# Kernel tuning notes

Measured on AMD Instinct MI355X. Metric: run time of the kernel, lower is better.

## Reference

```python
import jax, jax.numpy as jnp
import numpy as np

R = 16      # box filter radius (init kwarg)
EPS = 1e-4  # regularization (init kwarg)


def _diff_x(src, r):
    c = jnp.cumsum(src, axis=-2)
    left = c[..., r:2 * r + 1, :]
    middle = c[..., 2 * r + 1:, :] - c[..., :-2 * r - 1, :]
    right = c[..., -1:, :] - c[..., -2 * r - 1:-r - 1, :]
    return jnp.concatenate([left, middle, right], axis=-2)


def _diff_y(src, r):
    c = jnp.cumsum(src, axis=-1)
    left = c[..., r:2 * r + 1]
    middle = c[..., 2 * r + 1:] - c[..., :-2 * r - 1]
    right = c[..., -1:] - c[..., -2 * r - 1:-r - 1]
    return jnp.concatenate([left, middle, right], axis=-1)


def boxfilter2d(src, radius):
    return _diff_y(_diff_x(src, radius), radius)


def guidedfilter2d_color(guide, src, radius, eps):
    # guide: (B,3,H,W), src: (B,C,H,W)
    g_r, g_g, g_b = guide[:, 0:1], guide[:, 1:2], guide[:, 2:3]
    ones = jnp.ones_like(g_r)
    N = boxfilter2d(ones, radius)                       # (B,1,H,W)
    mean_I = boxfilter2d(guide, radius) / N             # (B,3,H,W)
    mI_r, mI_g, mI_b = mean_I[:, 0:1], mean_I[:, 1:2], mean_I[:, 2:3]
    mean_p = boxfilter2d(src, radius) / N               # (B,C,H,W)
    mean_Ip_r = boxfilter2d(g_r * src, radius) / N
    mean_Ip_g = boxfilter2d(g_g * src, radius) / N
    mean_Ip_b = boxfilter2d(g_b * src, radius) / N
    cov_Ip_r = mean_Ip_r - mI_r * mean_p
    cov_Ip_g = mean_Ip_g - mI_g * mean_p
    cov_Ip_b = mean_Ip_b - mI_b * mean_p
    v_rr = boxfilter2d(g_r * g_r, radius) / N - mI_r * mI_r + eps
    v_rg = boxfilter2d(g_r * g_g, radius) / N - mI_r * mI_g
    v_rb = boxfilter2d(g_r * g_b, radius) / N - mI_r * mI_b
    v_gg = boxfilter2d(g_g * g_g, radius) / N - mI_g * mI_g + eps
    v_gb = boxfilter2d(g_g * g_b, radius) / N - mI_g * mI_b
    v_bb = boxfilter2d(g_b * g_b, radius) / N - mI_b * mI_b + eps
    det = (v_rr * v_gg * v_bb + v_rg * v_gb * v_rb + v_rb * v_rg * v_gb
           - v_rb * v_gg * v_rb - v_rg * v_rg * v_bb - v_rr * v_gb * v_gb)
    i_rr = (v_gg * v_bb - v_gb * v_gb) / det
    i_rg = -(v_rg * v_bb - v_rb * v_gb) / det
    i_rb = (v_rg * v_gb - v_rb * v_gg) / det
    i_gg = (v_rr * v_bb - v_rb * v_rb) / det
    i_gb = -(v_rr * v_gb - v_rb * v_rg) / det
    i_bb = (v_rr * v_gg - v_rg * v_rg) / det
    # inv_sigma: (B,3,3,H,W) per-pixel inverse covariance
    inv_sigma = jnp.stack([
        jnp.stack([i_rr, i_rg, i_rb], axis=1),
        jnp.stack([i_rg, i_gg, i_gb], axis=1),
        jnp.stack([i_rb, i_gb, i_bb], axis=1)], axis=1)[..., 0, :, :]
    cov_Ip = jnp.stack([cov_Ip_r, cov_Ip_g, cov_Ip_b], axis=1)  # (B,3,C,H,W)
    a = jnp.einsum('bichw,bijhw->bjchw', cov_Ip, inv_sigma)     # (B,3,C,H,W)
    b = mean_p - a[:, 0] * mI_r - a[:, 1] * mI_g - a[:, 2] * mI_b
    mean_a = boxfilter2d(a, radius) / N[:, None]                # (B,3,C,H,W)
    mean_b = boxfilter2d(b, radius) / N
    q = jnp.einsum('bichw,bihw->bchw', mean_a, guide) + mean_b
    return q


def setup_inputs() -> dict:
    key = jax.random.key(0)
    k1, k2 = jax.random.split(key)
    guide = jax.random.uniform(k1, (1, 3, 2048, 2048), dtype=jnp.float32)
    src = jax.random.uniform(k2, (1, 3, 2048, 2048), dtype=jnp.float32)
    return {"guide": guide, "src": src}


def reference(guide, src):
    return guidedfilter2d_color(guide, src, R, EPS)
```

## Files before the change

### kernel.cpp

```cpp
#include <hip/hip_runtime.h>
#include <cstdio>
#include <cstdint>

#define HH 2048
#define WWI 2048
#define RAD 16
#define EPSF 1e-4f
#define BRA 16
#define BRB 32
#define W_OUT 94

typedef _Float16 h16;
constexpr size_t PLN = (size_t)HH * WWI;
constexpr int ROWB = WWI * 4;

__device__ __forceinline__ int cnt1d(int p, int n) {
    int lo = p - RAD; if (lo < 0) lo = 0;
    int hi = p + RAD; if (hi > n - 1) hi = n - 1;
    return hi - lo + 1;
}

__device__ __forceinline__ float ldf(const float* __restrict__ p, int boff) {
    return *reinterpret_cast<const float*>(reinterpret_cast<const char*>(p) + boff);
}
__device__ __forceinline__ float2 ldf2(const float* __restrict__ p, int boff) {
    return *reinterpret_cast<const float2*>(reinterpret_cast<const char*>(p) + boff);
}
__device__ __forceinline__ uint32_t ldu(const uint32_t* __restrict__ p, int boff) {
    return *reinterpret_cast<const uint32_t*>(reinterpret_cast<const char*>(p) + boff);
}
__device__ __forceinline__ void stu2(uint32_t* __restrict__ p, int boff, uint2 v) {
    *reinterpret_cast<uint2*>(reinterpret_cast<char*>(p) + boff) = v;
}
__device__ __forceinline__ void stf(float* __restrict__ p, int boff, float v) {
    *reinterpret_cast<float*>(reinterpret_cast<char*>(p) + boff) = v;
}
__device__ __forceinline__ uint32_t pk(float a, float b) {
    union { h16 h[2]; uint32_t u; } t;
    t.h[0] = (h16)a; t.h[1] = (h16)b; return t.u;
}
__device__ __forceinline__ float2 upk(uint32_t u) {
    union { uint32_t u; h16 h[2]; } t; t.u = u;
    return make_float2((float)t.h[0], (float)t.h[1]);
}

template<int CTRL, int RM>
__device__ __forceinline__ float dpp_add(float x) {
    int t = __builtin_amdgcn_update_dpp(0, __builtin_bit_cast(int, x), CTRL, RM, 0xf, false);
    return x + __builtin_bit_cast(float, t);
}
__device__ __forceinline__ float wscan(float x) {
    x = dpp_add<0x111, 0xf>(x);
    x = dpp_add<0x112, 0xf>(x);
    x = dpp_add<0x114, 0xf>(x);
    x = dpp_add<0x118, 0xf>(x);
    x = dpp_add<0x142, 0xa>(x);
    x = dpp_add<0x143, 0xc>(x);
    return x;
}
__device__ __forceinline__ float bperm(int byteaddr, float v) {
    return __builtin_bit_cast(float,
        __builtin_amdgcn_ds_bpermute(byteaddr, __builtin_bit_cast(int, v)));
}

template<bool ADD>
__device__ __forceinline__ void prod21(float v0, float v1, float v2,
                                       float v3, float v4, float v5, float S[21]) {
    float p[21];
    p[0] = v0; p[1] = v1; p[2] = v2; p[3] = v3; p[4] = v4; p[5] = v5;
    p[6] = v0 * v3; p[7] = v0 * v4; p[8] = v0 * v5;
    p[9] = v1 * v3; p[10] = v1 * v4; p[11] = v1 * v5;
    p[12] = v2 * v3; p[13] = v2 * v4; p[14] = v2 * v5;
    p[15] = v0 * v0; p[16] = v0 * v1; p[17] = v0 * v2;
    p[18] = v1 * v1; p[19] = v1 * v2; p[20] = v2 * v2;
#pragma unroll
    for (int c = 0; c < 21; ++c) { if constexpr (ADD) S[c] += p[c]; else S[c] -= p[c]; }
}

template<bool ADD>
__device__ __forceinline__ void acc21p(const float* __restrict__ g0, const float* __restrict__ g1,
                                       const float* __restrict__ g2, const float* __restrict__ s0,
                                       const float* __restrict__ s1, const float* __restrict__ s2,
                                       int boff, bool ok, float S0[21], float S1[21]) {
    if (!ok) return;
    const float2 a0 = ldf2(g0, boff), a1 = ldf2(g1, boff), a2 = ldf2(g2, boff);
    const float2 b0 = ldf2(s0, boff), b1 = ldf2(s1, boff), b2 = ldf2(s2, boff);
    prod21<ADD>(a0.x, a1.x, a2.x, b0.x, b1.x, b2.x, S0);
    prod21<ADD>(a0.y, a1.y, a2.y, b0.y, b1.y, b2.y, S1);
}

template<bool ADD>
__device__ __forceinline__ void acc12(const uint32_t* __restrict__ a0, const uint32_t* __restrict__ a1,
                                      const uint32_t* __restrict__ a2, const uint32_t* __restrict__ a3,
                                      const uint32_t* __restrict__ a4, const uint32_t* __restrict__ a5,
                                      int boff, bool ok, float S[12]) {
    if (!ok) return;
    const uint32_t u0 = ldu(a0, boff), u1 = ldu(a1, boff), u2 = ldu(a2, boff);
    const uint32_t u3 = ldu(a3, boff), u4 = ldu(a4, boff), u5 = ldu(a5, boff);
    const float2 f0 = upk(u0), f1 = upk(u1), f2 = upk(u2);
    const float2 f3 = upk(u3), f4 = upk(u4), f5 = upk(u5);
    if constexpr (ADD) {
        S[0] += f0.x; S[1] += f0.y; S[2] += f1.x; S[3] += f1.y;
        S[4] += f2.x; S[5] += f2.y; S[6] += f3.x; S[7] += f3.y;
        S[8] += f4.x; S[9] += f4.y; S[10] += f5.x; S[11] += f5.y;
    } else {
        S[0] -= f0.x; S[1] -= f0.y; S[2] -= f1.x; S[3] -= f1.y;
        S[4] -= f2.x; S[5] -= f2.y; S[6] -= f3.x; S[7] -= f3.y;
        S[8] -= f4.x; S[9] -= f4.y; S[10] -= f5.x; S[11] -= f5.y;
    }
}

__device__ __forceinline__ void solve_ab(const float S[21], float rN, float o[12]) {
    const float m0 = S[0] * rN, m1 = S[1] * rN, m2 = S[2] * rN;
    const float p0 = S[3] * rN, p1 = S[4] * rN, p2 = S[5] * rN;
    const float c00 = S[6] * rN - m0 * p0;
    const float c01 = S[7] * rN - m0 * p1;
    const float c02 = S[8] * rN - m0 * p2;
    const float c10 = S[9] * rN - m1 * p0;
    const float c11 = S[10] * rN - m1 * p1;
    const float c12 = S[11] * rN - m1 * p2;
    const float c20 = S[12] * rN - m2 * p0;
    const float c21 = S[13] * rN - m2 * p1;
    const float c22 = S[14] * rN - m2 * p2;
    const float vrr = S[15] * rN - m0 * m0 + EPSF;
    const float vrg = S[16] * rN - m0 * m1;
    const float vrb = S[17] * rN - m0 * m2;
    const float vgg = S[18] * rN - m1 * m1 + EPSF;
    const float vgb = S[19] * rN - m1 * m2;
    const float vbb = S[20] * rN - m2 * m2 + EPSF;
    const float det = vrr * vgg * vbb + vrg * vgb * vrb + vrb * vrg * vgb
                    - vrb * vgg * vrb - vrg * vrg * vbb - vrr * vgb * vgb;
    const float id = __builtin_amdgcn_rcpf(det);
    const float irr =  (vgg * vbb - vgb * vgb) * id;
    const float irg = -(vrg * vbb - vrb * vgb) * id;
    const float irb =  (vrg * vgb - vrb * vgg) * id;
    const float igg =  (vrr * vbb - vrb * vrb) * id;
    const float igb = -(vrr * vgb - vrb * vrg) * id;
    const float ibb =  (vrr * vgg - vrg * vrg) * id;
    const float a00 = c00 * irr + c10 * irg + c20 * irb;
    const float a01 = c01 * irr + c11 * irg + c21 * irb;
    const float a02 = c02 * irr + c12 * irg + c22 * irb;
    const float a10 = c00 * irg + c10 * igg + c20 * igb;
    const float a11 = c01 * irg + c11 * igg + c21 * igb;
    const float a12 = c02 * irg + c12 * igg + c22 * igb;
    const float a20 = c00 * irb + c10 * igb + c20 * ibb;
    const float a21 = c01 * irb + c11 * igb + c21 * ibb;
    const float a22 = c02 * irb + c12 * igb + c22 * ibb;
    o[0] = a00; o[1] = a01; o[2] = a02;
    o[3] = a10; o[4] = a11; o[5] = a12;
    o[6] = a20; o[7] = a21; o[8] = a22;
    o[9]  = p0 - a00 * m0 - a10 * m1 - a20 * m2;
    o[10] = p1 - a01 * m0 - a11 * m1 - a21 * m2;
    o[11] = p2 - a02 * m0 - a12 * m1 - a22 * m2;
}

#define LOAD6F(P, bo) { P[0] = ldf2(g0, bo); P[1] = ldf2(g1, bo); P[2] = ldf2(g2, bo); \
                        P[3] = ldf2(s0, bo); P[4] = ldf2(s1, bo); P[5] = ldf2(s2, bo); }
#define LOAD6U(P, bo) { P[0] = ldu(a0, bo); P[1] = ldu(a1, bo); P[2] = ldu(a2, bo); \
                        P[3] = ldu(a3, bo); P[4] = ldu(a4, bo); P[5] = ldu(a5, bo); }

__global__ __launch_bounds__(128, 3) void kA(const float* __restrict__ g,
                                             const float* __restrict__ s,
                                             uint32_t* __restrict__ ab) {
    const int lane = threadIdx.x & 63;
    const int wv   = blockIdx.x * 2 + (threadIdx.x >> 6);
    const int W0   = wv * W_OUT;
    const int X0   = W0 - 18;
    const int col0 = X0 + 2 * lane;
    const bool okc = (unsigned)col0 < (unsigned)WWI;
    const int r0   = blockIdx.y * BRA;
    const int aP17 = ((lane + 17) & 63) * 4;
    const int aP1  = ((lane + 1) & 63) * 4;
    const int j0   = W0 + 2 * lane;
    const bool outl = (lane <= 46) && (j0 < WWI);

    const float* g0 = g;         const float* g1 = g + PLN;   const float* g2 = g + 2 * PLN;
    const float* s0 = s;         const float* s1 = s + PLN;   const float* s2 = s + 2 * PLN;
    uint32_t* a0 = ab;           uint32_t* a1 = ab + PLN;     uint32_t* a2 = ab + 2 * PLN;
    uint32_t* a3 = ab + 3 * PLN; uint32_t* a4 = ab + 4 * PLN; uint32_t* a5 = ab + 5 * PLN;

    float S0[21], S1[21];
#pragma unroll
    for (int c = 0; c < 21; ++c) { S0[c] = 0.f; S1[c] = 0.f; }
    {
        int lo = r0 - RAD; if (lo < 0) lo = 0;
        int hi = r0 + RAD; if (hi > HH - 1) hi = HH - 1;
        int r = lo;
        if (okc) {
            int boff = lo * ROWB + col0 * 4;
            for (; r + 3 <= hi; r += 4) {
                float2 R0[6], R1[6], R2[6], R3[6];
                LOAD6F(R0, boff);
                LOAD6F(R1, boff + ROWB);
                LOAD6F(R2, boff + 2 * ROWB);
                LOAD6F(R3, boff + 3 * ROWB);
                prod21<true>(R0[0].x, R0[1].x, R0[2].x, R0[3].x, R0[4].x, R0[5].x, S0);
                prod21<true>(R0[0].y, R0[1].y, R0[2].y, R0[3].y, R0[4].y, R0[5].y, S1);
                prod21<true>(R1[0].x, R1[1].x, R1[2].x, R1[3].x, R1[4].x, R1[5].x, S0);
                prod21<true>(R1[0].y, R1[1].y, R1[2].y, R1[3].y, R1[4].y, R1[5].y, S1);
                prod21<true>(R2[0].x, R2[1].x, R2[2].x, R2[3].x, R2[4].x, R2[5].x, S0);
                prod21<true>(R2[0].y, R2[1].y, R2[2].y, R2[3].y, R2[4].y, R2[5].y, S1);
                prod21<true>(R3[0].x, R3[1].x, R3[2].x, R3[3].x, R3[4].x, R3[5].x, S0);
                prod21<true>(R3[0].y, R3[1].y, R3[2].y, R3[3].y, R3[4].y, R3[5].y, S1);
                boff += 4 * ROWB;
            }
            for (; r <= hi; ++r) {
                float2 R0[6];
                LOAD6F(R0, boff);
                prod21<true>(R0[0].x, R0[1].x, R0[2].x, R0[3].x, R0[4].x, R0[5].x, S0);
                prod21<true>(R0[0].y, R0[1].y, R0[2].y, R0[3].y, R0[4].y, R0[5].y, S1);
                boff += ROWB;
            }
        }
    }
    const float cx0 = (float)cnt1d(j0, WWI);
    const float cx1 = (float)cnt1d(j0 + 1, WWI);
    int raOff = (r0 + RAD + 1) * ROWB + col0 * 4;
    int rsOff = (r0 - RAD) * ROWB + col0 * 4;
    int oOff  = r0 * ROWB + j0 * 4;
    for (int ii = 0; ii < BRA; ++ii) {
        const int i = r0 + ii;
        float H0[21], H1[21];
#pragma unroll
        for (int c = 0; c < 21; ++c) {
            const float PP  = wscan(S0[c] + S1[c]);
            const float ppa = bperm(aP17, PP);
            const float s1b = bperm(aP17, S1[c]);
            const float s0b = bperm(aP1,  S0[c]);
            const float D = ppa - PP;
            H0[c] = D - s1b;
            H1[c] = D - s0b;
        }
        const float cy = (float)cnt1d(i, HH);
        float o0[12], o1[12];
        solve_ab(H0, __builtin_amdgcn_rcpf(cx0 * cy), o0);
        solve_ab(H1, __builtin_amdgcn_rcpf(cx1 * cy), o1);
        if (outl) {
            stu2(a0, oOff, make_uint2(pk(o0[0],  o0[1]),  pk(o1[0],  o1[1])));
            stu2(a1, oOff, make_uint2(pk(o0[2],  o0[3]),  pk(o1[2],  o1[3])));
            stu2(a2, oOff, make_uint2(pk(o0[4],  o0[5]),  pk(o1[4],  o1[5])));
            stu2(a3, oOff, make_uint2(pk(o0[6],  o0[7]),  pk(o1[6],  o1[7])));
            stu2(a4, oOff, make_uint2(pk(o0[8],  o0[9]),  pk(o1[8],  o1[9])));
            stu2(a5, oOff, make_uint2(pk(o0[10], o0[11]), pk(o1[10], o1[11])));
        }
        if (ii + 1 < BRA) {
            if (i + RAD + 1 < HH) acc21p<true >(g0, g1, g2, s0, s1, s2, raOff, okc, S0, S1);
            if (i - RAD >= 0)     acc21p<false>(g0, g1, g2, s0, s1, s2, rsOff, okc, S0, S1);
        }
        raOff += ROWB; rsOff += ROWB; oOff += ROWB;
    }
}

__global__ __launch_bounds__(256) void kB(const uint32_t* __restrict__ ab,
                                          const float* __restrict__ g,
                                          float* __restrict__ outp) {
    const int lane = threadIdx.x & 63;
    const int wv   = blockIdx.x * 4 + (threadIdx.x >> 6);
    const int x0   = wv * 32;
    const int col  = x0 - RAD + lane;
    const bool okc = (unsigned)col < (unsigned)WWI;
    const int colb = (okc ? col : 0) * 4;
    const int r0   = blockIdx.y * BRB;
    const int addrA = ((lane + 16) & 63) * 4;
    const int addrB = (lane >= 17 ? lane - 17 : 0) * 4;
    const bool subok = lane >= 17;
    const bool outl  = (lane >= 16) && (lane < 48);

    const uint32_t* a0 = ab;           const uint32_t* a1 = ab + PLN;     const uint32_t* a2 = ab + 2 * PLN;
    const uint32_t* a3 = ab + 3 * PLN; const uint32_t* a4 = ab + 4 * PLN; const uint32_t* a5 = ab + 5 * PLN;
    const float* g0 = g;  const float* g1 = g + PLN;  const float* g2 = g + 2 * PLN;
    float* o0 = outp;     float* o1 = outp + PLN;     float* o2 = outp + 2 * PLN;

    float S[12];
#pragma unroll
    for (int c = 0; c < 12; ++c) S[c] = 0.f;
    {
        int lo = r0 - RAD; if (lo < 0) lo = 0;
        int hi = r0 + RAD; if (hi > HH - 1) hi = HH - 1;
        int boff = lo * ROWB + col * 4;
        for (int r = lo; r <= hi; ++r) {
            acc12<true>(a0, a1, a2, a3, a4, a5, boff, okc, S);
            boff += ROWB;
        }
    }
    const float cx = (float)cnt1d(col, WWI);
    int oOff = r0 * ROWB + col * 4;

    uint32_t UA[6], UB[6], UA2[6], UB2[6];
    {
        const int boA = min(r0 + RAD + 1, HH - 1) * ROWB + colb;
        const int boB = max(r0 - RAD, 0) * ROWB + colb;
        LOAD6U(UA, boA);
        LOAD6U(UB, boB);
    }
    for (int ii = 0; ii < BRB; ++ii) {
        const int i = r0 + ii;
        if (ii + 1 < BRB) {
            const int boA = min(i + RAD + 2, HH - 1) * ROWB + colb;
            const int boB = max(i + 1 - RAD, 0) * ROWB + colb;
            LOAD6U(UA2, boA);
            LOAD6U(UB2, boB);
        }
        float H[12];
#pragma unroll
        for (int c = 0; c < 12; ++c) {
            const float sc = wscan(S[c]);
            const float hv = bperm(addrA, sc);
            const float lv = bperm(addrB, sc);
            H[c] = hv - (subok ? lv : 0.f);
        }
        if (ii + 1 < BRB) {
#pragma unroll
            for (int k = 0; k < 6; ++k) {
                UA[k] = okc ? UA[k] : 0u;
                UB[k] = okc ? UB[k] : 0u;
            }
            if (i + RAD + 1 < HH) {
#pragma unroll
                for (int k = 0; k < 6; ++k) {
                    const float2 f = upk(UA[k]);
                    S[2 * k] += f.x; S[2 * k + 1] += f.y;
                }
            }
            if (i - RAD >= 0) {
#pragma unroll
                for (int k = 0; k < 6; ++k) {
                    const float2 f = upk(UB[k]);
                    S[2 * k] -= f.x; S[2 * k + 1] -= f.y;
                }
            }
        }
        if (outl) {
            const float rN = __builtin_amdgcn_rcpf(cx * (float)cnt1d(i, HH));
            const float gg0 = ldf(g0, oOff), gg1 = ldf(g1, oOff), gg2 = ldf(g2, oOff);
            stf(o0, oOff, (H[0] * gg0 + H[3] * gg1 + H[6] * gg2 + H[9])  * rN);
            stf(o1, oOff, (H[1] * gg0 + H[4] * gg1 + H[7] * gg2 + H[10]) * rN);
            stf(o2, oOff, (H[2] * gg0 + H[5] * gg1 + H[8] * gg2 + H[11]) * rN);
        }
#pragma unroll
        for (int k = 0; k < 6; ++k) { UA[k] = UA2[k]; UB[k] = UB2[k]; }
        oOff += ROWB;
    }
}

extern "C" void kernel_launch(void* const* d_in, const int* in_sizes, int n_in,
                              void* d_out, int out_size, void* d_ws, size_t ws_size,
                              hipStream_t stream) {
    const float* g = (const float*)d_in[0];
    const float* s = (const float*)d_in[1];
    float* outp = (float*)d_out;
    uint32_t* ab = (uint32_t*)d_ws;

    const size_t need = 6 * PLN * sizeof(uint32_t);
    if (ws_size < need)
        fprintf(stderr, "[gf] WARNING ws_size=%zu < need=%zu\n", ws_size, need);

    kA<<<dim3(11, HH / BRA, 1), dim3(128, 1, 1), 0, stream>>>(g, s, ab);
    kB<<<dim3(WWI / 128, HH / BRB, 1), dim3(256, 1, 1), 0, stream>>>(ab, g, outp);
}
```

Baseline: 195.8 us.

## Prefetch sliding-window rows before scan and swizzle block order for XCD locality

In kA, the next add/subtract rows of guide and src are loaded at the top of each row iteration, so their global latency overlaps the wave-scan and permute work. Out-of-range reads are clamped and masked to zero rather than skipped by branching. Both kernels remap block IDs with an 8-way swizzle so that neighbouring tiles go to the same XCD, which is meant to improve L2 reuse of the overlapping halo rows. Occupancy for kA is raised from 3 to 4 blocks, which increases register pressure now that 24 prefetched values stay live across the scan.

```diff
diff --git a/kernel.cpp b/kernel.cpp
--- a/kernel.cpp
+++ b/kernel.cpp
@@ -75,18 +75,6 @@
     p[18] = v1 * v1; p[19] = v1 * v2; p[20] = v2 * v2;
 #pragma unroll
     for (int c = 0; c < 21; ++c) { if constexpr (ADD) S[c] += p[c]; else S[c] -= p[c]; }
-}
-
-template<bool ADD>
-__device__ __forceinline__ void acc21p(const float* __restrict__ g0, const float* __restrict__ g1,
-                                       const float* __restrict__ g2, const float* __restrict__ s0,
-                                       const float* __restrict__ s1, const float* __restrict__ s2,
-                                       int boff, bool ok, float S0[21], float S1[21]) {
-    if (!ok) return;
-    const float2 a0 = ldf2(g0, boff), a1 = ldf2(g1, boff), a2 = ldf2(g2, boff);
-    const float2 b0 = ldf2(s0, boff), b1 = ldf2(s1, boff), b2 = ldf2(s2, boff);
-    prod21<ADD>(a0.x, a1.x, a2.x, b0.x, b1.x, b2.x, S0);
-    prod21<ADD>(a0.y, a1.y, a2.y, b0.y, b1.y, b2.y, S1);
 }
 
 template<bool ADD>
@@ -159,16 +147,22 @@
 #define LOAD6U(P, bo) { P[0] = ldu(a0, bo); P[1] = ldu(a1, bo); P[2] = ldu(a2, bo); \
                         P[3] = ldu(a3, bo); P[4] = ldu(a4, bo); P[5] = ldu(a5, bo); }
 
-__global__ __launch_bounds__(128, 3) void kA(const float* __restrict__ g,
+__global__ __launch_bounds__(128, 4) void kA(const float* __restrict__ g,
                                              const float* __restrict__ s,
                                              uint32_t* __restrict__ ab) {
+    const int lid = blockIdx.y * 11 + blockIdx.x;
+    const int swz = (lid & 7) * 176 + (lid >> 3);
+    const int bx  = swz % 11;
+    const int by  = swz / 11;
+
     const int lane = threadIdx.x & 63;
-    const int wv   = blockIdx.x * 2 + (threadIdx.x >> 6);
+    const int wv   = bx * 2 + (threadIdx.x >> 6);
     const int W0   = wv * W_OUT;
     const int X0   = W0 - 18;
     const int col0 = X0 + 2 * lane;
     const bool okc = (unsigned)col0 < (unsigned)WWI;
-    const int r0   = blockIdx.y * BRA;
+    const int colb = (okc ? col0 : 0) * 4;
+    const int r0   = by * BRA;
     const int aP17 = ((lane + 17) & 63) * 4;
     const int aP1  = ((lane + 1) & 63) * 4;
     const int j0   = W0 + 2 * lane;
@@ -215,11 +209,17 @@
     }
     const float cx0 = (float)cnt1d(j0, WWI);
     const float cx1 = (float)cnt1d(j0 + 1, WWI);
-    int raOff = (r0 + RAD + 1) * ROWB + col0 * 4;
-    int rsOff = (r0 - RAD) * ROWB + col0 * 4;
-    int oOff  = r0 * ROWB + j0 * 4;
+    int oOff = r0 * ROWB + j0 * 4;
     for (int ii = 0; ii < BRA; ++ii) {
         const int i = r0 + ii;
+        float2 PA[6], PB[6];
+        const bool doAdv = (ii + 1 < BRA);
+        if (doAdv) {
+            const int boA = min(i + RAD + 1, HH - 1) * ROWB + colb;
+            const int boB = max(i - RAD, 0) * ROWB + colb;
+            LOAD6F(PA, boA);
+            LOAD6F(PB, boB);
+        }
         float H0[21], H1[21];
 #pragma unroll
         for (int c = 0; c < 21; ++c) {
@@ -230,6 +230,21 @@
             const float D = ppa - PP;
             H0[c] = D - s1b;
             H1[c] = D - s0b;
+        }
+        if (doAdv) {
+#pragma unroll
+            for (int k = 0; k < 6; ++k) {
+                PA[k].x = okc ? PA[k].x : 0.f; PA[k].y = okc ? PA[k].y : 0.f;
+                PB[k].x = okc ? PB[k].x : 0.f; PB[k].y = okc ? PB[k].y : 0.f;
+            }
+            if (i + RAD + 1 < HH) {
+                prod21<true>(PA[0].x, PA[1].x, PA[2].x, PA[3].x, PA[4].x, PA[5].x, S0);
+                prod21<true>(PA[0].y, PA[1].y, PA[2].y, PA[3].y, PA[4].y, PA[5].y, S1);
+            }
+            if (i - RAD >= 0) {
+                prod21<false>(PB[0].x, PB[1].x, PB[2].x, PB[3].x, PB[4].x, PB[5].x, S0);
+                prod21<false>(PB[0].y, PB[1].y, PB[2].y, PB[3].y, PB[4].y, PB[5].y, S1);
+            }
         }
         const float cy = (float)cnt1d(i, HH);
         float o0[12], o1[12];
@@ -243,24 +258,25 @@
             stu2(a4, oOff, make_uint2(pk(o0[8],  o0[9]),  pk(o1[8],  o1[9])));
             stu2(a5, oOff, make_uint2(pk(o0[10], o0[11]), pk(o1[10], o1[11])));
         }
-        if (ii + 1 < BRA) {
-            if (i + RAD + 1 < HH) acc21p<true >(g0, g1, g2, s0, s1, s2, raOff, okc, S0, S1);
-            if (i - RAD >= 0)     acc21p<false>(g0, g1, g2, s0, s1, s2, rsOff, okc, S0, S1);
-        }
-        raOff += ROWB; rsOff += ROWB; oOff += ROWB;
+        oOff += ROWB;
     }
 }
 
 __global__ __launch_bounds__(256) void kB(const uint32_t* __restrict__ ab,
                                           const float* __restrict__ g,
                                           float* __restrict__ outp) {
+    const int lid = blockIdx.y * 16 + blockIdx.x;
+    const int swz = (lid & 7) * 128 + (lid >> 3);
+    const int bx  = swz & 15;
+    const int by  = swz >> 4;
+
     const int lane = threadIdx.x & 63;
-    const int wv   = blockIdx.x * 4 + (threadIdx.x >> 6);
+    const int wv   = bx * 4 + (threadIdx.x >> 6);
     const int x0   = wv * 32;
     const int col  = x0 - RAD + lane;
     const bool okc = (unsigned)col < (unsigned)WWI;
     const int colb = (okc ? col : 0) * 4;
-    const int r0   = blockIdx.y * BRB;
+    const int r0   = by * BRB;
     const int addrA = ((lane + 16) & 63) * 4;
     const int addrB = (lane >= 17 ? lane - 17 : 0) * 4;
     const bool subok = lane >= 17;
```

Result: slower. 387.4 us (+97.8%).
